# Kernel optimization log

Measured on AMD Instinct MI355X. Metric: run time of the kernel, lower is better.

The kernel has to match this reference:

```python
import jax, jax.numpy as jnp
import numpy as np

B, T, G, D = 32, 120, 25, 256
H, HD = 8, 32  # H*HD == D
EPS = 1e-6


def _xavier(key, out_f, in_f):
    lim = float(np.sqrt(6.0 / (in_f + out_f)))
    return jax.random.uniform(key, (out_f, in_f), jnp.float32, -lim, lim)


def setup_inputs() -> dict:
    key = jax.random.key(0)
    ks = jax.random.split(key, 12)
    inp = {
        "x": jax.random.normal(ks[0], (B, T, G, D), jnp.float32),
        "adjacency_matrix": jax.random.uniform(ks[1], (G, G), jnp.float32),
        "Wq": _xavier(ks[2], H * HD, D), "bq": jnp.zeros((H * HD,), jnp.float32),
        "Wk": _xavier(ks[3], H * HD, D), "bk": jnp.zeros((H * HD,), jnp.float32),
        "Wv": _xavier(ks[4], H * HD, D), "bv": jnp.zeros((H * HD,), jnp.float32),
        "Wo": _xavier(ks[5], D, D), "bo": jnp.zeros((D,), jnp.float32),
        "Wfc": _xavier(ks[6], D, D), "bfc": jnp.zeros((D,), jnp.float32),
        "alpha": jnp.ones((D,), jnp.float32),
        "beta": jnp.zeros((D,), jnp.float32),
    }
    return inp


def _norm(z, alpha, beta):
    # torch: alpha * (x - mean) / (std(unbiased) + eps) + bias
    mu = jnp.mean(z, axis=-1, keepdims=True)
    sd = jnp.std(z, axis=-1, keepdims=True, ddof=1)
    return alpha * (z - mu) / (sd + EPS) + beta


def reference(x, adjacency_matrix, Wq, bq, Wk, bk, Wv, bv, Wo, bo, Wfc, bfc, alpha, beta):
    # adjacency aggregation: [G,G] @ [B,T,G,D] -> [B,T,G,D]
    h = jnp.einsum('gn,btnd->btgd', adjacency_matrix, x)

    def proj(W, b):
        # [B,T,G,D] -> [B,T,G,H,HD] -> transpose(1,2) -> [B,G,T,H,HD]
        p = (h @ W.T + b).reshape(B, T, G, H, HD)
        return jnp.swapaxes(p, 1, 2)

    Q, K, V = proj(Wq, bq), proj(Wk, bk), proj(Wv, bv)
    # scores over last two axes (H x H) -- faithful to the source's transpose quirk
    scores = (Q @ jnp.swapaxes(K, -2, -1)) / jnp.sqrt(jnp.float32(HD))  # [B,G,T,H,H]
    # F.softmax with no dim on a 5-D tensor -> torch softmaxes along dim=1 (G axis)
    w = jax.nn.softmax(scores, axis=1)
    att = w @ V  # [B,G,T,H,HD]
    att = jnp.swapaxes(att, 1, 2).reshape(B, T, G, D)
    x_att = att @ Wo.T + bo

    x1 = _norm(x + x_att, alpha, beta)
    x_fc = jax.nn.relu(x1 @ Wfc.T + bfc)
    return _norm(x1 + x_fc, alpha, beta)
```

## Files before the change

### kernel.cpp

```cpp
#include <hip/hip_runtime.h>

#define NB 32
#define NT 120
#define NG 25
#define ND 256
#define NH 8
#define NHD 32
#define NTH 512

typedef unsigned short u16;
typedef unsigned int u32;

typedef __bf16 bf16x8 __attribute__((ext_vector_type(8)));
typedef float  f32x4  __attribute__((ext_vector_type(4)));

#define SB 264
#define SF 268
#define OFF_HS_HI 0
#define OFF_HS_LO 16896
#define OFF_QKV   33792
#define OFF_ADJ   136704
#define OFF_SS    139312
#define OFF_WRED  145712
#define OFF_MU    146544
#define OFF_RSD   146656
#define SMEM_TOT  146768

#define WS_QKV_HI 0
#define WS_QKV_LO 196608
#define WS_WO_HI  393216
#define WS_WO_LO  458752
#define WS_WFC_HI 524288
#define WS_WFC_LO 589824
#define WS_NEED_BYTES (655360ull * 2ull)

__device__ __forceinline__ float bf2f(u16 u) { return __uint_as_float(((u32)u) << 16); }
__device__ __forceinline__ u16 f2bf(float f) {
    u32 x = __float_as_uint(f);
    return (u16)((x + 0x7FFFu + ((x >> 16) & 1u)) >> 16);
}
__device__ __forceinline__ void splitf(float v, u16& h, u16& l) {
    h = f2bf(v);
    l = f2bf(v - bf2f(h));
}
__device__ __forceinline__ bf16x8 ld_bf8(const u16* p) {
    uint4 u = *(const uint4*)p;
    return __builtin_bit_cast(bf16x8, u);
}

__global__ __launch_bounds__(256)
void prep_w(const float* __restrict__ Wq, const float* __restrict__ Wk,
            const float* __restrict__ Wv, const float* __restrict__ Wo,
            const float* __restrict__ Wfc, u16* __restrict__ ws) {
    int e = blockIdx.x * 256 + threadIdx.x;
    float v; int hi_base, lo_base, idx;
    if (e < 196608) {
        int n = e >> 8, k = e & 255;
        const float* W = (n < 256) ? Wq : (n < 512 ? Wk : Wv);
        v = W[(n & 255) * 256 + k];
        hi_base = WS_QKV_HI; lo_base = WS_QKV_LO; idx = e;
    } else if (e < 262144) {
        idx = e - 196608; v = Wo[idx];
        hi_base = WS_WO_HI; lo_base = WS_WO_LO;
    } else {
        idx = e - 262144; v = Wfc[idx];
        hi_base = WS_WFC_HI; lo_base = WS_WFC_LO;
    }
    u16 h, l; splitf(v, h, l);
    ws[hi_base + idx] = h;
    ws[lo_base + idx] = l;
}

__device__ __forceinline__ void norm_stats8(const float* zv, int g0, int gn,
                                            int lane, int wid, int tid,
                                            float (*s_wred)[13][2], float* s_mu, float* s_rsd) {
    (void)g0;
    #pragma unroll
    for (int i = 0; i < 13; ++i) {
        if (i >= gn) break;
        float s = zv[i], q = zv[i] * zv[i];
        #pragma unroll
        for (int off = 32; off > 0; off >>= 1) {
            s += __shfl_xor(s, off, 64);
            q += __shfl_xor(q, off, 64);
        }
        if (lane == 0) { s_wred[wid][i][0] = s; s_wred[wid][i][1] = q; }
    }
    __syncthreads();
    if (tid < NG) {
        const int g = tid;
        const int wb = (g < 13) ? 0 : 4, lg = (g < 13) ? g : g - 13;
        float s = 0.f, q = 0.f;
        #pragma unroll
        for (int w = 0; w < 4; ++w) { s += s_wred[wb + w][lg][0]; q += s_wred[wb + w][lg][1]; }
        float mu = s * (1.f / 256.f);
        float var = fmaxf((q - 256.f * mu * mu) * (1.f / 255.f), 0.f);
        s_mu[g] = mu;
        s_rsd[g] = 1.f / (sqrtf(var) + 1e-6f);
    }
    __syncthreads();
}

template<bool PREP>
__device__ __forceinline__ void load_bfrag(const u16* wshi, const u16* wslo,
                                           const float* Wf, int row, int koff,
                                           bf16x8& bh, bf16x8& bl) {
    if constexpr (PREP) {
        const int off = row * 256 + koff;
        bh = ld_bf8(wshi + off);
        bl = ld_bf8(wslo + off);
    } else {
        const float* p = Wf + row * 256 + koff;
        float4 w0 = *(const float4*)p, w1 = *(const float4*)(p + 4);
        float wv[8] = {w0.x, w0.y, w0.z, w0.w, w1.x, w1.y, w1.z, w1.w};
        union { u16 s[8]; bf16x8 v; } H, L;
        #pragma unroll
        for (int j = 0; j < 8; ++j) splitf(wv[j], H.s[j], L.s[j]);
        bh = H.v; bl = L.v;
    }
}

template<bool PREP>
__global__ __launch_bounds__(NTH, 2)
void enc_mfma(const float* __restrict__ x,  const float* __restrict__ adj,
              const float* __restrict__ Wq, const float* __restrict__ bq,
              const float* __restrict__ Wk, const float* __restrict__ bk,
              const float* __restrict__ Wv, const float* __restrict__ bv,
              const float* __restrict__ Wo, const float* __restrict__ bo,
              const float* __restrict__ Wfc,const float* __restrict__ bfc,
              const float* __restrict__ alpha, const float* __restrict__ beta,
              float* __restrict__ out, const u16* __restrict__ ws)
{
    extern __shared__ char smem[];
    u16*   hs_hi = (u16*)(smem + OFF_HS_HI);
    u16*   hs_lo = (u16*)(smem + OFF_HS_LO);
    float* qkvf  = (float*)(smem + OFF_QKV);
    float* adjf  = (float*)(smem + OFF_ADJ);
    float* ss    = (float*)(smem + OFF_SS);
    float (*s_wred)[13][2] = (float(*)[13][2])(smem + OFF_WRED);
    float* s_mu  = (float*)(smem + OFF_MU);
    float* s_rsd = (float*)(smem + OFF_RSD);

    const int bt = blockIdx.x;
    const int tid = threadIdx.x;
    const int d = tid & 255, rep = tid >> 8;
    const int lane = tid & 63, wid = tid >> 6;
    const int lm = lane & 15, quad = lane >> 4;
    const int g0 = rep ? 13 : 0, gn = rep ? 12 : 13;
    const long base = (long)bt * (NG * ND);

    for (int i = tid; i < NG * NG; i += NTH) adjf[i] = adj[i];
    __syncthreads();

    {
        float acc[13];
        #pragma unroll
        for (int i = 0; i < 13; ++i) acc[i] = 0.f;
        for (int n = 0; n < NG; ++n) {
            float xv = x[base + n * ND + d];
            #pragma unroll
            for (int i = 0; i < 13; ++i)
                acc[i] += adjf[(g0 + i) * NG + n] * xv;
        }
        #pragma unroll
        for (int i = 0; i < 13; ++i) {
            if (i >= gn) break;
            u16 h, l; splitf(acc[i], h, l);
            hs_hi[(g0 + i) * SB + d] = h; hs_lo[(g0 + i) * SB + d] = l;
        }
        if (rep) {
            #pragma unroll
            for (int g = NG; g < 32; ++g) { hs_hi[g * SB + d] = 0; hs_lo[g * SB + d] = 0; }
        }
    }
    __syncthreads();

    {
        f32x4 acc[2][6];
        #pragma unroll
        for (int mt = 0; mt < 2; ++mt)
            #pragma unroll
            for (int nt = 0; nt < 6; ++nt) acc[mt][nt] = (f32x4)0.f;

        for (int k0 = 0; k0 < 256; k0 += 32) {
            const int koff = k0 + quad * 8;
            bf16x8 ah[2], al[2];
            #pragma unroll
            for (int mt = 0; mt < 2; ++mt) {
                const int off = (mt * 16 + lm) * SB + koff;
                ah[mt] = ld_bf8(hs_hi + off);
                al[mt] = ld_bf8(hs_lo + off);
            }
            bf16x8 bh[6], bl[6];
            #pragma unroll
            for (int j = 0; j < 6; ++j) {
                const int n0 = wid * 96 + j * 16;
                const int mat = n0 >> 8;
                const float* Wf = (mat == 0) ? Wq : (mat == 1 ? Wk : Wv);
                load_bfrag<PREP>(ws + WS_QKV_HI, ws + WS_QKV_LO, Wf,
                                 PREP ? (n0 + lm) : ((n0 & 255) + lm), koff, bh[j], bl[j]);
            }
            #pragma unroll
            for (int j = 0; j < 6; ++j)
                #pragma unroll
                for (int mt = 0; mt < 2; ++mt)
                    acc[mt][j] = __builtin_amdgcn_mfma_f32_16x16x32_bf16(ah[mt], bh[j], acc[mt][j], 0, 0, 0);
            #pragma unroll
            for (int j = 0; j < 6; ++j)
                #pragma unroll
                for (int mt = 0; mt < 2; ++mt)
                    acc[mt][j] = __builtin_amdgcn_mfma_f32_16x16x32_bf16(al[mt], bh[j], acc[mt][j], 0, 0, 0);
            #pragma unroll
            for (int j = 0; j < 6; ++j)
                #pragma unroll
                for (int mt = 0; mt < 2; ++mt)
                    acc[mt][j] = __builtin_amdgcn_mfma_f32_16x16x32_bf16(ah[mt], bl[j], acc[mt][j], 0, 0, 0);
        }
        #pragma unroll
        for (int nt = 0; nt < 6; ++nt) {
            const int n0 = wid * 96 + nt * 16;
            const int mat = n0 >> 8, cb = (n0 & 255) + lm;
            const float* bp = (mat == 0) ? bq : (mat == 1 ? bk : bv);
            const float bb = bp[cb];
            float* plane = qkvf + mat * (32 * SF);
            #pragma unroll
            for (int mt = 0; mt < 2; ++mt)
                #pragma unroll
                for (int i = 0; i < 4; ++i)
                    plane[(mt * 16 + quad * 4 + i) * SF + cb] = acc[mt][nt][i] + bb;
        }
    }
    __syncthreads();

    for (int i = tid; i < NG * 64; i += NTH) {
        const int g = i >> 6, hh = i & 63;
        const float4* q4 = (const float4*)(qkvf + 0 * 32 * SF + g * SF + (hh >> 3) * NHD);
        const float4* k4 = (const float4*)(qkvf + 1 * 32 * SF + g * SF + (hh & 7) * NHD);
        float s = 0.f;
        #pragma unroll
        for (int c = 0; c < 8; ++c) {
            float4 qa = q4[c], ka = k4[c];
            s += qa.x * ka.x + qa.y * ka.y + qa.z * ka.z + qa.w * ka.w;
        }
        ss[i] = s * 0.17677669529663687f;
    }
    __syncthreads();

    {
        float* s_sm = adjf;
        const int col = tid & 63, part = tid >> 6;
        float m = -1e30f;
        for (int g = part; g < NG; g += 8) m = fmaxf(m, ss[g * 64 + col]);
        s_sm[part * 64 + col] = m;
        __syncthreads();
        float cm = -1e30f;
        #pragma unroll
        for (int p = 0; p < 8; ++p) cm = fmaxf(cm, s_sm[p * 64 + col]);
        __syncthreads();
        float den = 0.f;
        for (int g = part; g < NG; g += 8) {
            float e = expf(ss[g * 64 + col] - cm);
            ss[g * 64 + col] = e;
            den += e;
        }
        s_sm[part * 64 + col] = den;
        __syncthreads();
        float tden = 0.f;
        #pragma unroll
        for (int p = 0; p < 8; ++p) tden += s_sm[p * 64 + col];
        const float inv = 1.f / tden;
        for (int g = part; g < NG; g += 8) ss[g * 64 + col] *= inv;
    }
    __syncthreads();

    {
        const int h1 = (tid >> 5) & 7, hd = tid & 31;
        const float* Vp = qkvf + 2 * 32 * SF;
        #pragma unroll
        for (int i = 0; i < 13; ++i) {
            if (i >= gn) break;
            const int g = g0 + i;
            float a = 0.f;
            #pragma unroll
            for (int h2 = 0; h2 < NH; ++h2)
                a += ss[g * 64 + h1 * 8 + h2] * Vp[g * SF + h2 * NHD + hd];
            u16 h, l; splitf(a, h, l);
            hs_hi[g * SB + d] = h; hs_lo[g * SB + d] = l;
        }
    }
    __syncthreads();

    {
        f32x4 acc[2][2];
        #pragma unroll
        for (int mt = 0; mt < 2; ++mt)
            #pragma unroll
            for (int nt = 0; nt < 2; ++nt) acc[mt][nt] = (f32x4)0.f;

        for (int k0 = 0; k0 < 256; k0 += 32) {
            const int koff = k0 + quad * 8;
            bf16x8 ah[2], al[2];
            #pragma unroll
            for (int mt = 0; mt < 2; ++mt) {
                const int off = (mt * 16 + lm) * SB + koff;
                ah[mt] = ld_bf8(hs_hi + off);
                al[mt] = ld_bf8(hs_lo + off);
            }
            bf16x8 bh[2], bl[2];
            #pragma unroll
            for (int j = 0; j < 2; ++j)
                load_bfrag<PREP>(ws + WS_WO_HI, ws + WS_WO_LO, Wo,
                                 wid * 32 + j * 16 + lm, koff, bh[j], bl[j]);
            #pragma unroll
            for (int j = 0; j < 2; ++j)
                #pragma unroll
                for (int mt = 0; mt < 2; ++mt)
                    acc[mt][j] = __builtin_amdgcn_mfma_f32_16x16x32_bf16(ah[mt], bh[j], acc[mt][j], 0, 0, 0);
            #pragma unroll
            for (int j = 0; j < 2; ++j)
                #pragma unroll
                for (int mt = 0; mt < 2; ++mt)
                    acc[mt][j] = __builtin_amdgcn_mfma_f32_16x16x32_bf16(al[mt], bh[j], acc[mt][j], 0, 0, 0);
            #pragma unroll
            for (int j = 0; j < 2; ++j)
                #pragma unroll
                for (int mt = 0; mt < 2; ++mt)
                    acc[mt][j] = __builtin_amdgcn_mfma_f32_16x16x32_bf16(ah[mt], bl[j], acc[mt][j], 0, 0, 0);
        }
        float* zs = qkvf;
        #pragma unroll
        for (int nt = 0; nt < 2; ++nt) {
            const int col = wid * 32 + nt * 16 + lm;
            const float bb = bo[col];
            #pragma unroll
            for (int mt = 0; mt < 2; ++mt)
                #pragma unroll
                for (int i = 0; i < 4; ++i)
                    zs[(mt * 16 + quad * 4 + i) * SF + col] = acc[mt][nt][i] + bb;
        }
    }
    __syncthreads();

    float zv[13];
    {
        float* zs = qkvf;
        #pragma unroll
        for (int i = 0; i < 13; ++i) {
            if (i >= gn) break;
            zv[i] = zs[(g0 + i) * SF + d] + x[base + (g0 + i) * ND + d];
        }
    }
    norm_stats8(zv, g0, gn, lane, wid, tid, s_wred, s_mu, s_rsd);
    const float af = alpha[d], bef = beta[d];
    #pragma unroll
    for (int i = 0; i < 13; ++i) {
        if (i >= gn) break;
        const float x1 = af * (zv[i] - s_mu[g0 + i]) * s_rsd[g0 + i] + bef;
        zv[i] = x1;
        u16 h, l; splitf(x1, h, l);
        hs_hi[(g0 + i) * SB + d] = h; hs_lo[(g0 + i) * SB + d] = l;
    }
    __syncthreads();

    {
        f32x4 acc[2][2];
        #pragma unroll
        for (int mt = 0; mt < 2; ++mt)
            #pragma unroll
            for (int nt = 0; nt < 2; ++nt) acc[mt][nt] = (f32x4)0.f;

        for (int k0 = 0; k0 < 256; k0 += 32) {
            const int koff = k0 + quad * 8;
            bf16x8 ah[2], al[2];
            #pragma unroll
            for (int mt = 0; mt < 2; ++mt) {
                const int off = (mt * 16 + lm) * SB + koff;
                ah[mt] = ld_bf8(hs_hi + off);
                al[mt] = ld_bf8(hs_lo + off);
            }
            bf16x8 bh[2], bl[2];
            #pragma unroll
            for (int j = 0; j < 2; ++j)
                load_bfrag<PREP>(ws + WS_WFC_HI, ws + WS_WFC_LO, Wfc,
                                 wid * 32 + j * 16 + lm, koff, bh[j], bl[j]);
            #pragma unroll
            for (int j = 0; j < 2; ++j)
                #pragma unroll
                for (int mt = 0; mt < 2; ++mt)
                    acc[mt][j] = __builtin_amdgcn_mfma_f32_16x16x32_bf16(ah[mt], bh[j], acc[mt][j], 0, 0, 0);
            #pragma unroll
            for (int j = 0; j < 2; ++j)
                #pragma unroll
                for (int mt = 0; mt < 2; ++mt)
                    acc[mt][j] = __builtin_amdgcn_mfma_f32_16x16x32_bf16(al[mt], bh[j], acc[mt][j], 0, 0, 0);
            #pragma unroll
            for (int j = 0; j < 2; ++j)
                #pragma unroll
                for (int mt = 0; mt < 2; ++mt)
                    acc[mt][j] = __builtin_amdgcn_mfma_f32_16x16x32_bf16(ah[mt], bl[j], acc[mt][j], 0, 0, 0);
        }
        float* zs = qkvf;
        #pragma unroll
        for (int nt = 0; nt < 2; ++nt) {
            const int col = wid * 32 + nt * 16 + lm;
            const float bb = bfc[col];
            #pragma unroll
            for (int mt = 0; mt < 2; ++mt)
                #pragma unroll
                for (int i = 0; i < 4; ++i)
                    zs[(mt * 16 + quad * 4 + i) * SF + col] = fmaxf(acc[mt][nt][i] + bb, 0.f);
        }
    }
    __syncthreads();

    float z2[13];
    {
        float* zs = qkvf;
        #pragma unroll
        for (int i = 0; i < 13; ++i) {
            if (i >= gn) break;
            z2[i] = zv[i] + zs[(g0 + i) * SF + d];
        }
    }
    norm_stats8(z2, g0, gn, lane, wid, tid, s_wred, s_mu, s_rsd);
    #pragma unroll
    for (int i = 0; i < 13; ++i) {
        if (i >= gn) break;
        out[base + (g0 + i) * ND + d] = af * (z2[i] - s_mu[g0 + i]) * s_rsd[g0 + i] + bef;
    }
}

extern "C" void kernel_launch(void* const* d_in, const int* in_sizes, int n_in,
                              void* d_out, int out_size, void* d_ws, size_t ws_size,
                              hipStream_t stream) {
    (void)in_sizes; (void)n_in; (void)out_size;
    const float* x     = (const float*)d_in[0];
    const float* adj   = (const float*)d_in[1];
    const float* Wq    = (const float*)d_in[2];
    const float* bq    = (const float*)d_in[3];
    const float* Wk    = (const float*)d_in[4];
    const float* bk    = (const float*)d_in[5];
    const float* Wv    = (const float*)d_in[6];
    const float* bv    = (const float*)d_in[7];
    const float* Wo    = (const float*)d_in[8];
    const float* bo    = (const float*)d_in[9];
    const float* Wfc   = (const float*)d_in[10];
    const float* bfc   = (const float*)d_in[11];
    const float* alpha = (const float*)d_in[12];
    const float* beta  = (const float*)d_in[13];
    float* out = (float*)d_out;
    u16* ws = (u16*)d_ws;

    const bool prep = (ws_size >= WS_NEED_BYTES);

    hipFuncSetAttribute((const void*)enc_mfma<true>,
                        hipFuncAttributeMaxDynamicSharedMemorySize, SMEM_TOT);
    hipFuncSetAttribute((const void*)enc_mfma<false>,
                        hipFuncAttributeMaxDynamicSharedMemorySize, SMEM_TOT);

    if (prep) {
        prep_w<<<dim3(1280), dim3(256), 0, stream>>>(Wq, Wk, Wv, Wo, Wfc, ws);
        enc_mfma<true><<<dim3(NB * NT), dim3(NTH), SMEM_TOT, stream>>>(
            x, adj, Wq, bq, Wk, bk, Wv, bv, Wo, bo, Wfc, bfc, alpha, beta, out, ws);
    } else {
        enc_mfma<false><<<dim3(NB * NT), dim3(NTH), SMEM_TOT, stream>>>(
            x, adj, Wq, bq, Wk, bk, Wv, bv, Wo, bo, Wfc, bfc, alpha, beta, out, ws);
    }
}
```

Before: 1.028 ms.

## Double-buffer MFMA operand loads and prefetch weight fragments across barriers

The three GEMM loops are fully unrolled and double-buffered in registers. The A and B fragments for step k+1 are loaded before the MFMAs of step k run, and the first B fragment of each GEMM is issued before the preceding __syncthreads so global latency overlaps the barrier. The x values read in the adjacency stage are kept in registers to avoid reloading x for the residual, and the bias and alpha/beta loads are hoisted. The cost is much higher register pressure from the doubled 6-wide QKV fragment buffers, which could lower occupancy or cause spills.

```diff
diff --git a/kernel.cpp b/kernel.cpp
--- a/kernel.cpp
+++ b/kernel.cpp
@@ -71,10 +71,9 @@
     ws[lo_base + idx] = l;
 }
 
-__device__ __forceinline__ void norm_stats8(const float* zv, int g0, int gn,
+__device__ __forceinline__ void norm_stats8(const float* zv, int gn,
                                             int lane, int wid, int tid,
                                             float (*s_wred)[13][2], float* s_mu, float* s_rsd) {
-    (void)g0;
     #pragma unroll
     for (int i = 0; i < 13; ++i) {
         if (i >= gn) break;
@@ -149,15 +148,60 @@
     const int g0 = rep ? 13 : 0, gn = rep ? 12 : 13;
     const long base = (long)bt * (NG * ND);
 
+    auto loadA = [&](int k0, bf16x8 (&ah)[2], bf16x8 (&al)[2]) {
+        const int koff = k0 + quad * 8;
+        #pragma unroll
+        for (int mt = 0; mt < 2; ++mt) {
+            const int off = (mt * 16 + lm) * SB + koff;
+            ah[mt] = ld_bf8(hs_hi + off);
+            al[mt] = ld_bf8(hs_lo + off);
+        }
+    };
+    auto loadB_qkv = [&](int k0, bf16x8 (&bh)[6], bf16x8 (&bl)[6]) {
+        const int koff = k0 + quad * 8;
+        #pragma unroll
+        for (int j = 0; j < 6; ++j) {
+            const int n0 = wid * 96 + j * 16;
+            const int mat = n0 >> 8;
+            const float* Wf = (mat == 0) ? Wq : (mat == 1 ? Wk : Wv);
+            load_bfrag<PREP>(ws + WS_QKV_HI, ws + WS_QKV_LO, Wf,
+                             PREP ? (n0 + lm) : ((n0 & 255) + lm), koff, bh[j], bl[j]);
+        }
+    };
+    auto loadB_wo = [&](int k0, bf16x8 (&bh)[2], bf16x8 (&bl)[2]) {
+        const int koff = k0 + quad * 8;
+        #pragma unroll
+        for (int j = 0; j < 2; ++j)
+            load_bfrag<PREP>(ws + WS_WO_HI, ws + WS_WO_LO, Wo,
+                             wid * 32 + j * 16 + lm, koff, bh[j], bl[j]);
+    };
+    auto loadB_wfc = [&](int k0, bf16x8 (&bh)[2], bf16x8 (&bl)[2]) {
+        const int koff = k0 + quad * 8;
+        #pragma unroll
+        for (int j = 0; j < 2; ++j)
+            load_bfrag<PREP>(ws + WS_WFC_HI, ws + WS_WFC_LO, Wfc,
+                             wid * 32 + j * 16 + lm, koff, bh[j], bl[j]);
+    };
+
+    bf16x8 bh2[2][6], bl2[2][6];
+    bf16x8 bh6[2][2], bl6[2][2];
+    bf16x8 bh8[2][2], bl8[2][2];
+    float zx[13];
+    float zv[13];
+
     for (int i = tid; i < NG * NG; i += NTH) adjf[i] = adj[i];
+    const float af = alpha[d], bef = beta[d];
     __syncthreads();
 
     {
         float acc[13];
         #pragma unroll
         for (int i = 0; i < 13; ++i) acc[i] = 0.f;
+        #pragma unroll
         for (int n = 0; n < NG; ++n) {
             float xv = x[base + n * ND + d];
+            if (rep == 0) { if (n < 13) zx[n] = xv; }
+            else          { if (n >= 13) zx[n - 13] = xv; }
             #pragma unroll
             for (int i = 0; i < 13; ++i)
                 acc[i] += adjf[(g0 + i) * NG + n] * xv;
@@ -173,61 +217,59 @@
             for (int g = NG; g < 32; ++g) { hs_hi[g * SB + d] = 0; hs_lo[g * SB + d] = 0; }
         }
     }
-    __syncthreads();
-
-    {
-        f32x4 acc[2][6];
-        #pragma unroll
-        for (int mt = 0; mt < 2; ++mt)
-            #pragma unroll
-            for (int nt = 0; nt < 6; ++nt) acc[mt][nt] = (f32x4)0.f;
-
-        for (int k0 = 0; k0 < 256; k0 += 32) {
-            const int koff = k0 + quad * 8;
-            bf16x8 ah[2], al[2];
-            #pragma unroll
-            for (int mt = 0; mt < 2; ++mt) {
-                const int off = (mt * 16 + lm) * SB + koff;
-                ah[mt] = ld_bf8(hs_hi + off);
-                al[mt] = ld_bf8(hs_lo + off);
-            }
-            bf16x8 bh[6], bl[6];
-            #pragma unroll
-            for (int j = 0; j < 6; ++j) {
-                const int n0 = wid * 96 + j * 16;
-                const int mat = n0 >> 8;
-                const float* Wf = (mat == 0) ? Wq : (mat == 1 ? Wk : Wv);
-                load_bfrag<PREP>(ws + WS_QKV_HI, ws + WS_QKV_LO, Wf,
-                                 PREP ? (n0 + lm) : ((n0 & 255) + lm), koff, bh[j], bl[j]);
-            }
-            #pragma unroll
-            for (int j = 0; j < 6; ++j)
-                #pragma unroll
-                for (int mt = 0; mt < 2; ++mt)
-                    acc[mt][j] = __builtin_amdgcn_mfma_f32_16x16x32_bf16(ah[mt], bh[j], acc[mt][j], 0, 0, 0);
-            #pragma unroll
-            for (int j = 0; j < 6; ++j)
-                #pragma unroll
-                for (int mt = 0; mt < 2; ++mt)
-                    acc[mt][j] = __builtin_amdgcn_mfma_f32_16x16x32_bf16(al[mt], bh[j], acc[mt][j], 0, 0, 0);
-            #pragma unroll
-            for (int j = 0; j < 6; ++j)
-                #pragma unroll
-                for (int mt = 0; mt < 2; ++mt)
-                    acc[mt][j] = __builtin_amdgcn_mfma_f32_16x16x32_bf16(ah[mt], bl[j], acc[mt][j], 0, 0, 0);
-        }
+    loadB_qkv(0, bh2[0], bl2[0]);
+    __syncthreads();
+
+    {
+        float bb[6];
         #pragma unroll
         for (int nt = 0; nt < 6; ++nt) {
             const int n0 = wid * 96 + nt * 16;
             const int mat = n0 >> 8, cb = (n0 & 255) + lm;
             const float* bp = (mat == 0) ? bq : (mat == 1 ? bk : bv);
-            const float bb = bp[cb];
+            bb[nt] = bp[cb];
+        }
+        f32x4 acc[2][6];
+        #pragma unroll
+        for (int mt = 0; mt < 2; ++mt)
+            #pragma unroll
+            for (int nt = 0; nt < 6; ++nt) acc[mt][nt] = (f32x4)0.f;
+
+        bf16x8 ah[2][2], al[2][2];
+        loadA(0, ah[0], al[0]);
+        #pragma unroll
+        for (int ki = 0; ki < 8; ++ki) {
+            const int cur = ki & 1, nxt = cur ^ 1;
+            if (ki < 7) {
+                loadB_qkv(32 * (ki + 1), bh2[nxt], bl2[nxt]);
+                loadA(32 * (ki + 1), ah[nxt], al[nxt]);
+            }
+            #pragma unroll
+            for (int j = 0; j < 6; ++j)
+                #pragma unroll
+                for (int mt = 0; mt < 2; ++mt)
+                    acc[mt][j] = __builtin_amdgcn_mfma_f32_16x16x32_bf16(ah[cur][mt], bh2[cur][j], acc[mt][j], 0, 0, 0);
+            #pragma unroll
+            for (int j = 0; j < 6; ++j)
+                #pragma unroll
+                for (int mt = 0; mt < 2; ++mt)
+                    acc[mt][j] = __builtin_amdgcn_mfma_f32_16x16x32_bf16(al[cur][mt], bh2[cur][j], acc[mt][j], 0, 0, 0);
+            #pragma unroll
+            for (int j = 0; j < 6; ++j)
+                #pragma unroll
+                for (int mt = 0; mt < 2; ++mt)
+                    acc[mt][j] = __builtin_amdgcn_mfma_f32_16x16x32_bf16(ah[cur][mt], bl2[cur][j], acc[mt][j], 0, 0, 0);
+        }
+        #pragma unroll
+        for (int nt = 0; nt < 6; ++nt) {
+            const int n0 = wid * 96 + nt * 16;
+            const int mat = n0 >> 8, cb = (n0 & 255) + lm;
             float* plane = qkvf + mat * (32 * SF);
             #pragma unroll
             for (int mt = 0; mt < 2; ++mt)
                 #pragma unroll
                 for (int i = 0; i < 4; ++i)
-                    plane[(mt * 16 + quad * 4 + i) * SF + cb] = acc[mt][nt][i] + bb;
+                    plane[(mt * 16 + quad * 4 + i) * SF + cb] = acc[mt][nt][i] + bb[nt];
         }
     }
     __syncthreads();
@@ -288,70 +330,64 @@
             hs_hi[g * SB + d] = h; hs_lo[g * SB + d] = l;
         }
     }
-    __syncthreads();
-
-    {
+    loadB_wo(0, bh6[0], bl6[0]);
+    __syncthreads();
+
+    {
+        float bb[2] = { bo[wid * 32 + lm], bo[wid * 32 + 16 + lm] };
         f32x4 acc[2][2];
         #pragma unroll
         for (int mt = 0; mt < 2; ++mt)
             #pragma unroll
             for (int nt = 0; nt < 2; ++nt) acc[mt][nt] = (f32x4)0.f;
 
-        for (int k0 = 0; k0 < 256; k0 += 32) {
-            const int koff = k0 + quad * 8;
-            bf16x8 ah[2], al[2];
-            #pragma unroll
-            for (int mt = 0; mt < 2; ++mt) {
-                const int off = (mt * 16 + lm) * SB + koff;
-                ah[mt] = ld_bf8(hs_hi + off);
-                al[mt] = ld_bf8(hs_lo + off);
+        bf16x8 ah[2][2], al[2][2];
+        loadA(0, ah[0], al[0]);
+        #pragma unroll
+        for (int ki = 0; ki < 8; ++ki) {
+            const int cur = ki & 1, nxt = cur ^ 1;
+            if (ki < 7) {
+                loadB_wo(32 * (ki + 1), bh6[nxt], bl6[nxt]);
+                loadA(32 * (ki + 1), ah[nxt], al[nxt]);
             }
-            bf16x8 bh[2], bl[2];
             #pragma unroll
             for (int j = 0; j < 2; ++j)
-                load_bfrag<PREP>(ws + WS_WO_HI, ws + WS_WO_LO, Wo,
-                                 wid * 32 + j * 16 + lm, koff, bh[j], bl[j]);
+                #pragma unroll
+                for (int mt = 0; mt < 2; ++mt)
+                    acc[mt][j] = __builtin_amdgcn_mfma_f32_16x16x32_bf16(ah[cur][mt], bh6[cur][j], acc[mt][j], 0, 0, 0);
             #pragma unroll
             for (int j = 0; j < 2; ++j)
                 #pragma unroll
                 for (int mt = 0; mt < 2; ++mt)
-                    acc[mt][j] = __builtin_amdgcn_mfma_f32_16x16x32_bf16(ah[mt], bh[j], acc[mt][j], 0, 0, 0);
+                    acc[mt][j] = __builtin_amdgcn_mfma_f32_16x16x32_bf16(al[cur][mt], bh6[cur][j], acc[mt][j], 0, 0, 0);
             #pragma unroll
             for (int j = 0; j < 2; ++j)
                 #pragma unroll
                 for (int mt = 0; mt < 2; ++mt)
-                    acc[mt][j] = __builtin_amdgcn_mfma_f32_16x16x32_bf16(al[mt], bh[j], acc[mt][j], 0, 0, 0);
-            #pragma unroll
-            for (int j = 0; j < 2; ++j)
-                #pragma unroll
-                for (int mt = 0; mt < 2; ++mt)
-                    acc[mt][j] = __builtin_amdgcn_mfma_f32_16x16x32_bf16(ah[mt], bl[j], acc[mt][j], 0, 0, 0);
+                    acc[mt][j] = __builtin_amdgcn_mfma_f32_16x16x32_bf16(ah[cur][mt], bl6[cur][j], acc[mt][j], 0, 0, 0);
         }
         float* zs = qkvf;
         #pragma unroll
         for (int nt = 0; nt < 2; ++nt) {
             const int col = wid * 32 + nt * 16 + lm;
-            const float bb = bo[col];
             #pragma unroll
             for (int mt = 0; mt < 2; ++mt)
                 #pragma unroll
                 for (int i = 0; i < 4; ++i)
-                    zs[(mt * 16 + quad * 4 + i) * SF + col] = acc[mt][nt][i] + bb;
-        }
-    }
-    __syncthreads();
-
-    float zv[13];
+                    zs[(mt * 16 + quad * 4 + i) * SF + col] = acc[mt][nt][i] + bb[nt];
+        }
+    }
+    __syncthreads();
+
     {
         float* zs = qkvf;
         #pragma unroll
         for (int i = 0; i < 13; ++i) {
             if (i >= gn) break;
-            zv[i] = zs[(g0 + i) * SF + d] + x[base + (g0 + i) * ND + d];
-        }
-    }
-    norm_stats8(zv, g0, gn, lane, wid, tid, s_wred, s_mu, s_rsd);
-    const float af = alpha[d], bef = beta[d];
+            zv[i] = zs[(g0 + i) * SF + d] + zx[i];
+        }
+    }
+    norm_stats8(zv, gn, lane, wid, tid, s_wred, s_mu, s_rsd);
     #pragma unroll
     for (int i = 0; i < 13; ++i) {
         if (i >= gn) break;
@@ -360,55 +396,51 @@
         u16 h, l; splitf(x1, h, l);
         hs_hi[(g0 + i) * SB + d] = h; hs_lo[(g0 + i) * SB + d] = l;
     }
-    __syncthreads();
-
-    {
+    loadB_wfc(0, bh8[0], bl8[0]);
+    __syncthreads();
+
+    {
+        float bb[2] = { bfc[wid * 32 + lm], bfc[wid * 32 + 16 + lm] };
         f32x4 acc[2][2];
         #pragma unroll
         for (int mt = 0; mt < 2; ++mt)
             #pragma unroll
             for (int nt = 0; nt < 2; ++nt) acc[mt][nt] = (f32x4)0.f;
 
-        for (int k0 = 0; k0 < 256; k0 += 32) {
-            const int koff = k0 + quad * 8;
-            bf16x8 ah[2], al[2];
-            #pragma unroll
-            for (int mt = 0; mt < 2; ++mt) {
-                const int off = (mt * 16 + lm) * SB + koff;
-                ah[mt] = ld_bf8(hs_hi + off);
-                al[mt] = ld_bf8(hs_lo + off);
+        bf16x8 ah[2][2], al[2][2];
+        loadA(0, ah[0], al[0]);
+        #pragma unroll
+        for (int ki = 0; ki < 8; ++ki) {
+            const int cur = ki & 1, nxt = cur ^ 1;
+            if (ki < 7) {
+                loadB_wfc(32 * (ki + 1), bh8[nxt], bl8[nxt]);
+                loadA(32 * (ki + 1), ah[nxt], al[nxt]);
             }
-            bf16x8 bh[2], bl[2];
             #pragma unroll
             for (int j = 0; j < 2; ++j)
-                load_bfrag<PREP>(ws + WS_WFC_HI, ws + WS_WFC_LO, Wfc,
-                                 wid * 32 + j * 16 + lm, koff, bh[j], bl[j]);
+                #pragma unroll
+                for (int mt = 0; mt < 2; ++mt)
+                    acc[mt][j] = __builtin_amdgcn_mfma_f32_16x16x32_bf16(ah[cur][mt], bh8[cur][j], acc[mt][j], 0, 0, 0);
             #pragma unroll
             for (int j = 0; j < 2; ++j)
                 #pragma unroll
                 for (int mt = 0; mt < 2; ++mt)
-                    acc[mt][j] = __builtin_amdgcn_mfma_f32_16x16x32_bf16(ah[mt], bh[j], acc[mt][j], 0, 0, 0);
+                    acc[mt][j] = __builtin_amdgcn_mfma_f32_16x16x32_bf16(al[cur][mt], bh8[cur][j], acc[mt][j], 0, 0, 0);
             #pragma unroll
             for (int j = 0; j < 2; ++j)
                 #pragma unroll
                 for (int mt = 0; mt < 2; ++mt)
-                    acc[mt][j] = __builtin_amdgcn_mfma_f32_16x16x32_bf16(al[mt], bh[j], acc[mt][j], 0, 0, 0);
-            #pragma unroll
-            for (int j = 0; j < 2; ++j)
-                #pragma unroll
-                for (int mt = 0; mt < 2; ++mt)
-                    acc[mt][j] = __builtin_amdgcn_mfma_f32_16x16x32_bf16(ah[mt], bl[j], acc[mt][j], 0, 0, 0);
+                    acc[mt][j] = __builtin_amdgcn_mfma_f32_16x16x32_bf16(ah[cur][mt], bl8[cur][j], acc[mt][j], 0, 0, 0);
         }
         float* zs = qkvf;
         #pragma unroll
         for (int nt = 0; nt < 2; ++nt) {
             const int col = wid * 32 + nt * 16 + lm;
-            const float bb = bfc[col];
             #pragma unroll
             for (int mt = 0; mt < 2; ++mt)
                 #pragma unroll
                 for (int i = 0; i < 4; ++i)
-                    zs[(mt * 16 + quad * 4 + i) * SF + col] = fmaxf(acc[mt][nt][i] + bb, 0.f);
+                    zs[(mt * 16 + quad * 4 + i) * SF + col] = fmaxf(acc[mt][nt][i] + bb[nt], 0.f);
         }
     }
     __syncthreads();
@@ -422,7 +454,7 @@
             z2[i] = zv[i] + zs[(g0 + i) * SF + d];
         }
     }
-    norm_stats8(z2, g0, gn, lane, wid, tid, s_wred, s_mu, s_rsd);
+    norm_stats8(z2, gn, lane, wid, tid, s_wred, s_mu, s_rsd);
     #pragma unroll
     for (int i = 0; i < 13; ++i) {
         if (i >= gn) break;
```

New measurement: 983.9 us. 1.04x faster.
